# Kernel tuning notes

Measured on AMD Instinct MI355X. Metric: run time of the kernel, lower is better.

## Reference

```python
import jax, jax.numpy as jnp
import numpy as np

B, N, D = 8, 512, 1024
E, H, TOP_K = 8, 8, 2
HD = D // H
EPS = 1e-5


def setup_inputs() -> dict:
    key = jax.random.key(0)
    ks = jax.random.split(key, 8)
    # kaiming_uniform with a=sqrt(5) over fan_in=N -> bound = sqrt(6/((1+5)*N)) = 1/sqrt(N)
    bound_w = 1.0 / np.sqrt(N)
    bound_lin = 1.0 / np.sqrt(D)
    return {
        "x": jax.random.normal(ks[0], (B, N, D), dtype=jnp.float32),
        "weight": jax.random.uniform(ks[1], (E, H, N, N), jnp.float32, -bound_w, bound_w),
        "bias": jnp.zeros((E, H, N), jnp.float32),
        "router_w": jax.random.uniform(ks[2], (E, D), jnp.float32, -bound_lin, bound_lin),
        "in_w": jax.random.uniform(ks[3], (D, D), jnp.float32, -bound_lin, bound_lin),
        "in_b": jax.random.uniform(ks[4], (D,), jnp.float32, -bound_lin, bound_lin),
        "out_w": jax.random.uniform(ks[5], (D, D), jnp.float32, -bound_lin, bound_lin),
        "out_b": jax.random.uniform(ks[6], (D,), jnp.float32, -bound_lin, bound_lin),
    }


def reference(x, weight, bias, router_w, in_w, in_b, out_w, out_b):
    # Router: mean-pool tokens, linear, softmax, top-k
    router_logits = x.mean(axis=1) @ router_w.T              # (B, E)
    router_probs = jax.nn.softmax(router_logits, axis=-1)
    top_w, top_i = jax.lax.top_k(router_probs, TOP_K)        # (B, K)
    top_w = top_w / top_w.sum(axis=-1, keepdims=True)

    # Input projection -> (B, H, hd, N), layer-norm over token axis N (no affine)
    xp = x @ in_w.T + in_b                                   # (B, N, D)
    xr = xp.reshape(B, N, H, HD).transpose(0, 2, 3, 1)       # (B, H, hd, N)
    mu = xr.mean(axis=-1, keepdims=True)
    var = xr.var(axis=-1, keepdims=True)
    xn = (xr - mu) * jax.lax.rsqrt(var + EPS)

    # Gather per-(batch, head, k) NxN expert matrices, row-softmax
    w = weight[top_i].transpose(0, 2, 1, 3, 4)               # (B, H, K, N, N)
    b = bias[top_i].transpose(0, 2, 1, 3)                    # (B, H, K, N)
    w_attn = jax.nn.softmax(w, axis=-1)

    # out[b,h,k,d,m] = sum_n xn[b,h,d,n] * w_attn[b,h,k,m,n]
    out = jnp.einsum('bhdn,bhkmn->bhkdm', xn, w_attn)
    out = out + b[:, :, :, None, :]                          # (B, H, K, hd, N)
    out = (out * top_w[:, None, :, None, None]).sum(axis=2)  # (B, H, hd, N)

    out = out.transpose(0, 3, 1, 2).reshape(B, N, D)         # (B, N, D)
    out = out @ out_w.T + out_b

    # Load-balancing aux loss
    top1 = top_i[:, 0]
    expert_mask = jax.nn.one_hot(top1, E, dtype=jnp.float32)
    aux = E * (router_probs.mean(axis=0) * expert_mask.mean(axis=0)).sum()
    return out, aux
```

## Files before the change

### kernel.cpp

```cpp
#include <hip/hip_runtime.h>
#include <hip/hip_bf16.h>

#define Bv 8
#define Nv 512
#define Dv 1024
#define Ev 8
#define Hv 8
#define HDv 128
#define EPSv 1e-5f

typedef __attribute__((ext_vector_type(8))) short short8;
typedef __attribute__((ext_vector_type(4))) float f32x4;

__device__ __forceinline__ unsigned short f2b(float f) {
    __hip_bfloat16 h = __float2bfloat16(f);
    return *reinterpret_cast<unsigned short*>(&h);
}
__device__ __forceinline__ float bf2f(unsigned int u) {
    union { unsigned int i; float f; } v; v.i = u << 16; return v.f;
}

__device__ __forceinline__ void gld16(const void* g, void* l) {
    __builtin_amdgcn_global_load_lds(
        (const __attribute__((address_space(1))) void*)(uintptr_t)(g),
        (__attribute__((address_space(3))) void*)(uintptr_t)(l), 16, 0, 0);
}

__global__ __launch_bounds__(256) void k_pre(const float* __restrict__ x,
                                             const float* __restrict__ weight,
                                             const float* __restrict__ w1,
                                             const float* __restrict__ w2,
                                             unsigned short* __restrict__ xb,
                                             float* __restrict__ part_x,
                                             float2* __restrict__ rstat,
                                             unsigned short* __restrict__ w1b,
                                             unsigned short* __restrict__ w2b) {
    int bid = blockIdx.x;
    int t = threadIdx.x;
    if (bid < 2048) {
        int lane = t & 63;
        int r0 = bid * 16 + (t >> 6) * 4;
        const float* wp = weight + (size_t)r0 * Nv + lane * 8;
        float4 va[4][2];
        #pragma unroll
        for (int r = 0; r < 4; ++r) {
            va[r][0] = *(const float4*)(wp + (size_t)r * Nv);
            va[r][1] = *(const float4*)(wp + (size_t)r * Nv + 4);
        }
        float mx[4], sm[4];
        #pragma unroll
        for (int r = 0; r < 4; ++r) {
            float4 a = va[r][0], b = va[r][1];
            mx[r] = fmaxf(fmaxf(fmaxf(a.x, a.y), fmaxf(a.z, a.w)),
                          fmaxf(fmaxf(b.x, b.y), fmaxf(b.z, b.w)));
        }
        for (int off = 1; off < 64; off <<= 1) {
            #pragma unroll
            for (int r = 0; r < 4; ++r) mx[r] = fmaxf(mx[r], __shfl_xor(mx[r], off));
        }
        #pragma unroll
        for (int r = 0; r < 4; ++r) {
            float4 a = va[r][0], b = va[r][1];
            sm[r] = __expf(a.x - mx[r]) + __expf(a.y - mx[r])
                  + __expf(a.z - mx[r]) + __expf(a.w - mx[r])
                  + __expf(b.x - mx[r]) + __expf(b.y - mx[r])
                  + __expf(b.z - mx[r]) + __expf(b.w - mx[r]);
        }
        for (int off = 1; off < 64; off <<= 1) {
            #pragma unroll
            for (int r = 0; r < 4; ++r) sm[r] += __shfl_xor(sm[r], off);
        }
        if (lane == 0) {
            #pragma unroll
            for (int r = 0; r < 4; ++r)
                rstat[r0 + r] = make_float2(mx[r], 1.f / sm[r]);
        }
        return;
    }
    if (bid < 2048 + 128) {
        int xb2 = bid - 2048;
        int b = xb2 >> 4, c = xb2 & 15;
        const float* px = x + ((size_t)b * Nv + c * 32) * Dv + t * 4;
        unsigned short* qx = xb + ((size_t)b * Nv + c * 32) * Dv + t * 4;
        float4 s4 = make_float4(0.f, 0.f, 0.f, 0.f);
        #pragma unroll 8
        for (int r = 0; r < 32; ++r) {
            float4 v = *(const float4*)(px + (size_t)r * Dv);
            s4.x += v.x; s4.y += v.y; s4.z += v.z; s4.w += v.w;
            uint2 pk;
            pk.x = (unsigned)f2b(v.x) | ((unsigned)f2b(v.y) << 16);
            pk.y = (unsigned)f2b(v.z) | ((unsigned)f2b(v.w) << 16);
            *(uint2*)(qx + (size_t)r * Dv) = pk;
        }
        *(float4*)(part_x + ((size_t)(b * 16 + c)) * Dv + t * 4) = s4;
        return;
    }
    int c = (bid - 2176) * 256 + t;
    const float* src; unsigned short* dst; int off;
    if (c < 131072) { src = w1; dst = w1b; off = c; }
    else            { src = w2; dst = w2b; off = c - 131072; }
    float4 a = ((const float4*)src)[off * 2];
    float4 b = ((const float4*)src)[off * 2 + 1];
    union { unsigned short h[8]; uint4 u; } pk;
    pk.h[0] = f2b(a.x); pk.h[1] = f2b(a.y); pk.h[2] = f2b(a.z); pk.h[3] = f2b(a.w);
    pk.h[4] = f2b(b.x); pk.h[5] = f2b(b.y); pk.h[6] = f2b(b.z); pk.h[7] = f2b(b.w);
    ((uint4*)dst)[off] = pk.u;
}

template <int MODE>
__global__ __launch_bounds__(256) void k_gemm(
    const unsigned short* __restrict__ A,
    const unsigned short* __restrict__ W,
    const float* __restrict__ bias,
    void* __restrict__ Cv,
    float2* __restrict__ part,
    const float* __restrict__ part_x,
    float* __restrict__ xmean,
    int M, int Nn, int K) {
    __shared__ __align__(16) unsigned short sA[3][128 * 64];
    __shared__ __align__(16) unsigned short sB[3][128 * 64];
    const int t = threadIdx.x;
    const int bn = blockIdx.x * 128;
    const int bm = blockIdx.y * 128;
    const int lane = t & 63;
    const int w = t >> 6, wm = w >> 1, wn = w & 1;
    const int fr = lane & 15, fq = lane >> 4;
    const int NT = K >> 6;
    f32x4 acc[4][4] = {};

#define STAGE(s, k0)                                                        \
    {                                                                       \
        _Pragma("unroll")                                                   \
        for (int i_ = 0; i_ < 4; ++i_) {                                    \
            int c_ = t + i_ * 256;                                          \
            int row_ = c_ >> 3, col_ = c_ & 7;                              \
            int cs_ = col_ ^ (row_ & 7);                                    \
            gld16(A + (size_t)(bm + row_) * K + (k0) + cs_ * 8, &sA[s][c_ * 8]); \
            gld16(W + (size_t)(bn + row_) * K + (k0) + cs_ * 8, &sB[s][c_ * 8]); \
        }                                                                   \
    }

    STAGE(0, 0);
    STAGE(1, 64);
    if (MODE == 2) {
        int blk = blockIdx.y * 8 + blockIdx.x;
        int o = blk * 32 + (t >> 3);
        int c2 = t & 7;
        int b2 = o >> 10, d2 = o & 1023;
        float S = part_x[((size_t)(b2 * 16 + c2)) * Dv + d2]
                + part_x[((size_t)(b2 * 16 + c2 + 8)) * Dv + d2];
        S += __shfl_xor(S, 1); S += __shfl_xor(S, 2); S += __shfl_xor(S, 4);
        if (c2 == 0) xmean[o] = S * (1.f / Nv);
    }
    for (int it = 0; it < NT; ++it) {
        if (it + 2 < NT) {
            STAGE((it + 2) % 3, (it + 2) * 64);
            asm volatile("s_waitcnt vmcnt(16)" ::: "memory");
        } else if (it + 1 < NT) {
            asm volatile("s_waitcnt vmcnt(8)" ::: "memory");
        } else {
            asm volatile("s_waitcnt vmcnt(0)" ::: "memory");
        }
        __builtin_amdgcn_s_barrier();
        const unsigned short* pA = sA[it % 3];
        const unsigned short* pB = sB[it % 3];
        #pragma unroll
        for (int kk = 0; kk < 2; ++kk) {
            short8 af[4], bv[4];
            #pragma unroll
            for (int i = 0; i < 4; ++i)
                af[i] = *(const short8*)&pA[(wm * 64 + i * 16 + fr) * 64 + (((kk << 2) + fq) ^ (fr & 7)) * 8];
            #pragma unroll
            for (int j = 0; j < 4; ++j)
                bv[j] = *(const short8*)&pB[(wn * 64 + j * 16 + fr) * 64 + (((kk << 2) + fq) ^ (fr & 7)) * 8];
            #pragma unroll
            for (int i = 0; i < 4; ++i)
                #pragma unroll
                for (int j = 0; j < 4; ++j)
                    acc[i][j] = __builtin_amdgcn_mfma_f32_16x16x32_bf16(af[i], bv[j], acc[i][j], 0, 0, 0);
        }
        __builtin_amdgcn_s_barrier();
    }
#undef STAGE
    if (MODE == 0) {
        #pragma unroll
        for (int j = 0; j < 4; ++j) {
            const int n = bn + wn * 64 + j * 16 + fr;
            const float bj = bias[n];
            #pragma unroll
            for (int i = 0; i < 4; ++i) {
                const int m0 = bm + wm * 64 + i * 16 + fq * 4;
                #pragma unroll
                for (int r = 0; r < 4; ++r)
                    ((float*)Cv)[(size_t)(m0 + r) * Nn + n] = acc[i][j][r] + bj;
            }
        }
    } else {
        unsigned short* sc = &sA[0][0];
        float2* red = (float2*)&sB[0][0];
        const int bB   = bm >> 9;
        const int tok0 = bm & 511;
        const int chunk = (bm >> 7) & 3;
        #pragma unroll
        for (int j = 0; j < 4; ++j) {
            const int col = wn * 64 + j * 16 + fr;
            const float bj = bias[bn + col];
            float s = 0.f, q = 0.f;
            #pragma unroll
            for (int i = 0; i < 4; ++i) {
                const int row0 = wm * 64 + i * 16 + fq * 4;
                #pragma unroll
                for (int r = 0; r < 4; r += 2) {
                    float v0 = acc[i][j][r] + bj;
                    float v1 = acc[i][j][r + 1] + bj;
                    s += v0 + v1;
                    q = fmaf(v0, v0, fmaf(v1, v1, q));
                    unsigned int pk = (unsigned int)f2b(v0) | ((unsigned int)f2b(v1) << 16);
                    *(unsigned int*)&sc[col * 136 + row0 + r] = pk;
                }
            }
            red[col * 8 + wm * 4 + fq] = make_float2(s, q);
        }
        __syncthreads();
        if (t < 128) {
            float S = 0.f, Q = 0.f;
            #pragma unroll
            for (int k = 0; k < 8; ++k) { float2 v = red[t * 8 + k]; S += v.x; Q += v.y; }
            part[((size_t)bB * Dv + bn + t) * 4 + chunk] = make_float2(S, Q);
        }
        unsigned short* dst = (unsigned short*)Cv;
        #pragma unroll
        for (int k = 0; k < 8; ++k) {
            const int c = t + k * 256;
            const int dl = c >> 4, tk = c & 15;
            uint4 v = *(const uint4*)&sc[dl * 136 + tk * 8];
            *(uint4*)&dst[((size_t)bB * Dv + bn + dl) * Nv + tok0 + tk * 8] = v;
        }
    }
}

__global__ __launch_bounds__(256) void k_mixg(
    const float* __restrict__ weight,
    const float2* __restrict__ rstat,
    const unsigned short* __restrict__ xpT,
    const float* __restrict__ bias,
    const float* __restrict__ xmean,
    const float* __restrict__ router_w,
    const float2* __restrict__ part,
    unsigned short* __restrict__ y,
    float* __restrict__ aux_out) {
    __shared__ __align__(16) unsigned short sA[2][128 * 64];
    __shared__ __align__(16) unsigned short sB[2][128 * 64];
    __shared__ float probs[Bv][Ev];
    __shared__ float twsh[Bv][2];
    __shared__ int   tsel[Bv][2];
    __shared__ int   top1s[Bv];
    const int t = threadIdx.x;
    const int bm = blockIdx.x * 128;
    const int bh = blockIdx.y;
    const int b = bh >> 3, h = bh & 7;

    {
        int pid = t >> 2, l = t & 3;
        int rb = pid >> 3, re = pid & 7;
        const float4* xm = (const float4*)(xmean + rb * Dv);
        const float4* rw = (const float4*)(router_w + re * Dv);
        float s = 0.f;
        #pragma unroll
        for (int j = 0; j < 64; ++j) {
            float4 aa = xm[l + j * 4], ww = rw[l + j * 4];
            s = fmaf(aa.x, ww.x, s); s = fmaf(aa.y, ww.y, s);
            s = fmaf(aa.z, ww.z, s); s = fmaf(aa.w, ww.w, s);
        }
        s += __shfl_xor(s, 1); s += __shfl_xor(s, 2);
        if (l == 0) probs[rb][re] = s;
    }
    __syncthreads();
    if (t < Bv) {
        int bb = t;
        float mx = -1e30f;
        for (int e2 = 0; e2 < Ev; ++e2) mx = fmaxf(mx, probs[bb][e2]);
        float sum = 0.f;
        for (int e2 = 0; e2 < Ev; ++e2) { float v = __expf(probs[bb][e2] - mx); probs[bb][e2] = v; sum += v; }
        float inv = 1.f / sum;
        for (int e2 = 0; e2 < Ev; ++e2) probs[bb][e2] *= inv;
        int i0 = 0; float p0 = probs[bb][0];
        for (int e2 = 1; e2 < Ev; ++e2) if (probs[bb][e2] > p0) { p0 = probs[bb][e2]; i0 = e2; }
        int i1 = -1; float p1 = -1.f;
        for (int e2 = 0; e2 < Ev; ++e2) if (e2 != i0 && probs[bb][e2] > p1) { p1 = probs[bb][e2]; i1 = e2; }
        float s2 = p0 + p1;
        tsel[bb][0] = i0; tsel[bb][1] = i1;
        twsh[bb][0] = p0 / s2; twsh[bb][1] = p1 / s2;
        top1s[bb] = i0;
    }
    __syncthreads();
    if (blockIdx.x == 0 && bh == 0 && t == 0) {
        float aux = 0.f;
        for (int e2 = 0; e2 < Ev; ++e2) {
            float pm = 0.f, mm = 0.f;
            for (int bb = 0; bb < Bv; ++bb) { pm += probs[bb][e2]; mm += (top1s[bb] == e2) ? 1.f : 0.f; }
            aux += (pm / Bv) * (mm / Bv);
        }
        *aux_out = aux * Ev;
    }
    const int e0 = tsel[b][0], e1 = tsel[b][1];
    const float tw0 = twsh[b][0], tw1 = twsh[b][1];

    const int lane = t & 63;
    const int w = t >> 6, wm = w >> 1, wn = w & 1;
    const int fr = lane & 15, fq = lane >> 4;

    float rstd_j[4], nmr_j[4];
    #pragma unroll
    for (int j = 0; j < 4; ++j) {
        const int dg = h * HDv + wn * 64 + j * 16 + fr;
        const float2* pp = part + ((size_t)b * Dv + dg) * 4;
        float S = 0.f, Q = 0.f;
        #pragma unroll
        for (int cc = 0; cc < 4; ++cc) { float2 v = pp[cc]; S += v.x; Q += v.y; }
        float mu = S * (1.f / Nv);
        float var = Q * (1.f / Nv) - mu * mu;
        float rs = rsqrtf(var + EPSv);
        rstd_j[j] = rs; nmr_j[j] = -mu * rs;
    }

    const float* W0 = weight + (size_t)(e0 * Hv + h) * Nv * Nv;
    const float* W1 = weight + (size_t)(e1 * Hv + h) * Nv * Nv;
    const float2* R0 = rstat + (size_t)(e0 * Hv + h) * Nv;
    const float2* R1 = rstat + (size_t)(e1 * Hv + h) * Nv;
    const unsigned short* Bb = xpT + ((size_t)b * Dv + h * HDv) * Nv;

    float m0s[4], c0s[4], m1s[4], c1s[4];
    #pragma unroll
    for (int i = 0; i < 4; ++i) {
        int rg = bm + (t >> 3) + i * 32;
        float2 s0 = R0[rg], s1 = R1[rg];
        m0s[i] = s0.x; c0s[i] = tw0 * s0.y;
        m1s[i] = s1.x; c1s[i] = tw1 * s1.y;
    }

    const int NT = Nv >> 6;
    f32x4 acc[4][4] = {};
    float4 ra0[4][2], ra1[4][2];

#define BSTAGE(s, k0)                                                       \
    {                                                                       \
        _Pragma("unroll")                                                   \
        for (int i_ = 0; i_ < 4; ++i_) {                                    \
            int c_ = t + i_ * 256;                                          \
            int row_ = c_ >> 3, col_ = c_ & 7;                              \
            int cs_ = col_ ^ (row_ & 7);                                    \
            gld16(Bb + (size_t)row_ * Nv + (k0) + cs_ * 8, &sB[s][c_ * 8]); \
        }                                                                   \
    }
#define ALOAD(k0)                                                           \
    {                                                                       \
        _Pragma("unroll")                                                   \
        for (int i_ = 0; i_ < 4; ++i_) {                                    \
            int c_ = t + i_ * 256;                                          \
            int row_ = c_ >> 3, col_ = c_ & 7;                              \
            int cs_ = col_ ^ (row_ & 7);                                    \
            size_t off_ = (size_t)(bm + row_) * Nv + (k0) + cs_ * 8;        \
            ra0[i_][0] = *(const float4*)&W0[off_];                         \
            ra0[i_][1] = *(const float4*)&W0[off_ + 4];                     \
            ra1[i_][0] = *(const float4*)&W1[off_];                         \
            ra1[i_][1] = *(const float4*)&W1[off_ + 4];                     \
        }                                                                   \
    }

    BSTAGE(0, 0);
    ALOAD(0);
    for (int it = 0; it < NT; ++it) {
        if (it + 1 < NT) {
            BSTAGE((it + 1) & 1, (it + 1) * 64);
            asm volatile("s_waitcnt vmcnt(4)" ::: "memory");
        } else {
            asm volatile("s_waitcnt vmcnt(0)" ::: "memory");
        }
        #pragma unroll
        for (int i = 0; i < 4; ++i) {
            int c = t + i * 256;
            float o[8];
            const float4 a0 = ra0[i][0], a1 = ra0[i][1];
            const float4 b0 = ra1[i][0], b1 = ra1[i][1];
            o[0] = c0s[i] * __expf(a0.x - m0s[i]) + c1s[i] * __expf(b0.x - m1s[i]);
            o[1] = c0s[i] * __expf(a0.y - m0s[i]) + c1s[i] * __expf(b0.y - m1s[i]);
            o[2] = c0s[i] * __expf(a0.z - m0s[i]) + c1s[i] * __expf(b0.z - m1s[i]);
            o[3] = c0s[i] * __expf(a0.w - m0s[i]) + c1s[i] * __expf(b0.w - m1s[i]);
            o[4] = c0s[i] * __expf(a1.x - m0s[i]) + c1s[i] * __expf(b1.x - m1s[i]);
            o[5] = c0s[i] * __expf(a1.y - m0s[i]) + c1s[i] * __expf(b1.y - m1s[i]);
            o[6] = c0s[i] * __expf(a1.z - m0s[i]) + c1s[i] * __expf(b1.z - m1s[i]);
            o[7] = c0s[i] * __expf(a1.w - m0s[i]) + c1s[i] * __expf(b1.w - m1s[i]);
            uint4 pk;
            pk.x = (unsigned)f2b(o[0]) | ((unsigned)f2b(o[1]) << 16);
            pk.y = (unsigned)f2b(o[2]) | ((unsigned)f2b(o[3]) << 16);
            pk.z = (unsigned)f2b(o[4]) | ((unsigned)f2b(o[5]) << 16);
            pk.w = (unsigned)f2b(o[6]) | ((unsigned)f2b(o[7]) << 16);
            *(uint4*)&sA[it & 1][c * 8] = pk;
        }
        if (it + 1 < NT) ALOAD((it + 1) * 64);
        asm volatile("s_waitcnt lgkmcnt(0)" ::: "memory");
        __builtin_amdgcn_s_barrier();
        const unsigned short* pA = sA[it & 1];
        const unsigned short* pB = sB[it & 1];
        #pragma unroll
        for (int kk = 0; kk < 2; ++kk) {
            short8 af[4], bv[4];
            #pragma unroll
            for (int i = 0; i < 4; ++i)
                af[i] = *(const short8*)&pA[(wm * 64 + i * 16 + fr) * 64 + (((kk << 2) + fq) ^ (fr & 7)) * 8];
            #pragma unroll
            for (int j = 0; j < 4; ++j)
                bv[j] = *(const short8*)&pB[(wn * 64 + j * 16 + fr) * 64 + (((kk << 2) + fq) ^ (fr & 7)) * 8];
            #pragma unroll
            for (int i = 0; i < 4; ++i)
                #pragma unroll
                for (int j = 0; j < 4; ++j)
                    acc[i][j] = __builtin_amdgcn_mfma_f32_16x16x32_bf16(af[i], bv[j], acc[i][j], 0, 0, 0);
        }
        __builtin_amdgcn_s_barrier();
    }
#undef BSTAGE
#undef ALOAD
    #pragma unroll
    for (int i = 0; i < 4; ++i) {
        #pragma unroll
        for (int r = 0; r < 4; ++r) {
            const int m = bm + wm * 64 + i * 16 + fq * 4 + r;
            const float br = tw0 * bias[(size_t)(e0 * Hv + h) * Nv + m]
                           + tw1 * bias[(size_t)(e1 * Hv + h) * Nv + m];
            #pragma unroll
            for (int j = 0; j < 4; ++j) {
                const int d = wn * 64 + j * 16 + fr;
                float v = fmaf(acc[i][j][r], rstd_j[j], nmr_j[j] + br);
                y[((size_t)b * Nv + m) * Dv + h * HDv + d] = f2b(v);
            }
        }
    }
}

extern "C" void kernel_launch(void* const* d_in, const int* in_sizes, int n_in,
                              void* d_out, int out_size, void* d_ws, size_t ws_size,
                              hipStream_t stream) {
    const float* x        = (const float*)d_in[0];
    const float* weight   = (const float*)d_in[1];
    const float* bias     = (const float*)d_in[2];
    const float* router_w = (const float*)d_in[3];
    const float* in_w     = (const float*)d_in[4];
    const float* in_b     = (const float*)d_in[5];
    const float* out_w    = (const float*)d_in[6];
    const float* out_b    = (const float*)d_in[7];
    float* out = (float*)d_out;

    if (ws_size < ((size_t)63 << 20)) return;

    char* wsb = (char*)d_ws;
    float*  xmean  = (float*)(wsb);
    float2* part   = (float2*)(wsb + (64 << 10));
    float*  part_x = (float*)(wsb + (512 << 10));
    float2* rstat  = (float2*)(wsb + ((size_t)1 << 20));
    unsigned short* in_wb  = (unsigned short*)(wsb + ((size_t)2 << 20));
    unsigned short* out_wb = (unsigned short*)(wsb + ((size_t)4 << 20));
    unsigned short* xb     = (unsigned short*)(wsb + ((size_t)8 << 20));
    unsigned short* xpT    = (unsigned short*)(wsb + ((size_t)16 << 20));
    unsigned short* y = xb;

    k_pre<<<3200, 256, 0, stream>>>(x, weight, in_w, out_w, xb, part_x, rstat, in_wb, out_wb);
    k_gemm<2><<<dim3(8, 32), 256, 0, stream>>>(xb, in_wb, in_b, xpT, part, part_x, xmean,
                                               Bv * Nv, Dv, Dv);
    k_mixg<<<dim3(4, 64), 256, 0, stream>>>(weight, rstat, xpT, bias, xmean, router_w, part, y,
                                            out + (size_t)Bv * Nv * Dv);
    k_gemm<0><<<dim3(8, 32), 256, 0, stream>>>(y, out_wb, out_b, out, nullptr, nullptr, nullptr,
                                               Bv * Nv, Dv, Dv);
}
```

Baseline: 76.93 us.

## Compute expert softmax row sums in-kernel only for selected experts, drop max pass

The pre-pass no longer computes softmax statistics over all 64 expert/head weight matrices. Each mixing block now computes row sums of exp(w) itself, and only for the two routed experts of its batch. Because the weights are bounded small values, the max subtraction is dropped. This removes reading the full 32 MB weight tensor in the pre-kernel. In exchange each mixing block reads its weight rows twice, and the missing max shift means the softmax could overflow for arbitrary weights. The weight-conversion blocks are also restructured so each block converts larger contiguous chunks.

```diff
diff --git a/kernel.cpp b/kernel.cpp
--- a/kernel.cpp
+++ b/kernel.cpp
@@ -26,60 +26,17 @@
         (__attribute__((address_space(3))) void*)(uintptr_t)(l), 16, 0, 0);
 }
 
-__global__ __launch_bounds__(256) void k_pre(const float* __restrict__ x,
-                                             const float* __restrict__ weight,
-                                             const float* __restrict__ w1,
-                                             const float* __restrict__ w2,
-                                             unsigned short* __restrict__ xb,
-                                             float* __restrict__ part_x,
-                                             float2* __restrict__ rstat,
-                                             unsigned short* __restrict__ w1b,
-                                             unsigned short* __restrict__ w2b) {
+__global__ __launch_bounds__(256) void k_preA(const float* __restrict__ x,
+                                              const float* __restrict__ w1,
+                                              const float* __restrict__ w2,
+                                              unsigned short* __restrict__ xb,
+                                              float* __restrict__ part_x,
+                                              unsigned short* __restrict__ w1b,
+                                              unsigned short* __restrict__ w2b) {
     int bid = blockIdx.x;
     int t = threadIdx.x;
-    if (bid < 2048) {
-        int lane = t & 63;
-        int r0 = bid * 16 + (t >> 6) * 4;
-        const float* wp = weight + (size_t)r0 * Nv + lane * 8;
-        float4 va[4][2];
-        #pragma unroll
-        for (int r = 0; r < 4; ++r) {
-            va[r][0] = *(const float4*)(wp + (size_t)r * Nv);
-            va[r][1] = *(const float4*)(wp + (size_t)r * Nv + 4);
-        }
-        float mx[4], sm[4];
-        #pragma unroll
-        for (int r = 0; r < 4; ++r) {
-            float4 a = va[r][0], b = va[r][1];
-            mx[r] = fmaxf(fmaxf(fmaxf(a.x, a.y), fmaxf(a.z, a.w)),
-                          fmaxf(fmaxf(b.x, b.y), fmaxf(b.z, b.w)));
-        }
-        for (int off = 1; off < 64; off <<= 1) {
-            #pragma unroll
-            for (int r = 0; r < 4; ++r) mx[r] = fmaxf(mx[r], __shfl_xor(mx[r], off));
-        }
-        #pragma unroll
-        for (int r = 0; r < 4; ++r) {
-            float4 a = va[r][0], b = va[r][1];
-            sm[r] = __expf(a.x - mx[r]) + __expf(a.y - mx[r])
-                  + __expf(a.z - mx[r]) + __expf(a.w - mx[r])
-                  + __expf(b.x - mx[r]) + __expf(b.y - mx[r])
-                  + __expf(b.z - mx[r]) + __expf(b.w - mx[r]);
-        }
-        for (int off = 1; off < 64; off <<= 1) {
-            #pragma unroll
-            for (int r = 0; r < 4; ++r) sm[r] += __shfl_xor(sm[r], off);
-        }
-        if (lane == 0) {
-            #pragma unroll
-            for (int r = 0; r < 4; ++r)
-                rstat[r0 + r] = make_float2(mx[r], 1.f / sm[r]);
-        }
-        return;
-    }
-    if (bid < 2048 + 128) {
-        int xb2 = bid - 2048;
-        int b = xb2 >> 4, c = xb2 & 15;
+    if (bid < 128) {
+        int b = bid >> 4, c = bid & 15;
         const float* px = x + ((size_t)b * Nv + c * 32) * Dv + t * 4;
         unsigned short* qx = xb + ((size_t)b * Nv + c * 32) * Dv + t * 4;
         float4 s4 = make_float4(0.f, 0.f, 0.f, 0.f);
@@ -95,16 +52,17 @@
         *(float4*)(part_x + ((size_t)(b * 16 + c)) * Dv + t * 4) = s4;
         return;
     }
-    int c = (bid - 2176) * 256 + t;
-    const float* src; unsigned short* dst; int off;
-    if (c < 131072) { src = w1; dst = w1b; off = c; }
-    else            { src = w2; dst = w2b; off = c - 131072; }
-    float4 a = ((const float4*)src)[off * 2];
-    float4 b = ((const float4*)src)[off * 2 + 1];
-    union { unsigned short h[8]; uint4 u; } pk;
-    pk.h[0] = f2b(a.x); pk.h[1] = f2b(a.y); pk.h[2] = f2b(a.z); pk.h[3] = f2b(a.w);
-    pk.h[4] = f2b(b.x); pk.h[5] = f2b(b.y); pk.h[6] = f2b(b.z); pk.h[7] = f2b(b.w);
-    ((uint4*)dst)[off] = pk.u;
+    const float* src; unsigned short* dst; int base;
+    if (bid < 256) { src = w1; dst = w1b; base = (bid - 128) * 8192; }
+    else           { src = w2; dst = w2b; base = (bid - 256) * 8192; }
+    #pragma unroll
+    for (int i = 0; i < 8; ++i) {
+        float4 a = *(const float4*)(src + base + i * 1024 + t * 4);
+        uint2 p;
+        p.x = (unsigned)f2b(a.x) | ((unsigned)f2b(a.y) << 16);
+        p.y = (unsigned)f2b(a.z) | ((unsigned)f2b(a.w) << 16);
+        *(uint2*)(dst + base + i * 1024 + t * 4) = p;
+    }
 }
 
 template <int MODE>
@@ -241,7 +199,6 @@
 
 __global__ __launch_bounds__(256) void k_mixg(
     const float* __restrict__ weight,
-    const float2* __restrict__ rstat,
     const unsigned short* __restrict__ xpT,
     const float* __restrict__ bias,
     const float* __restrict__ xmean,
@@ -326,17 +283,38 @@
 
     const float* W0 = weight + (size_t)(e0 * Hv + h) * Nv * Nv;
     const float* W1 = weight + (size_t)(e1 * Hv + h) * Nv * Nv;
-    const float2* R0 = rstat + (size_t)(e0 * Hv + h) * Nv;
-    const float2* R1 = rstat + (size_t)(e1 * Hv + h) * Nv;
     const unsigned short* Bb = xpT + ((size_t)b * Dv + h * HDv) * Nv;
 
-    float m0s[4], c0s[4], m1s[4], c1s[4];
-    #pragma unroll
-    for (int i = 0; i < 4; ++i) {
-        int rg = bm + (t >> 3) + i * 32;
-        float2 s0 = R0[rg], s1 = R1[rg];
-        m0s[i] = s0.x; c0s[i] = tw0 * s0.y;
-        m1s[i] = s1.x; c1s[i] = tw1 * s1.y;
+    float c0s[4], c1s[4];
+    {
+        float s0a[4] = {0.f, 0.f, 0.f, 0.f}, s1a[4] = {0.f, 0.f, 0.f, 0.f};
+        for (int k0 = 0; k0 < Nv; k0 += 64) {
+            #pragma unroll
+            for (int i = 0; i < 4; ++i) {
+                int c = t + i * 256;
+                int row = c >> 3, col = c & 7;
+                int cs = col ^ (row & 7);
+                size_t off = (size_t)(bm + row) * Nv + k0 + cs * 8;
+                float4 a0 = *(const float4*)&W0[off];
+                float4 a1 = *(const float4*)&W0[off + 4];
+                float4 b0 = *(const float4*)&W1[off];
+                float4 b1 = *(const float4*)&W1[off + 4];
+                s0a[i] += ((__expf(a0.x) + __expf(a0.y)) + (__expf(a0.z) + __expf(a0.w)))
+                        + ((__expf(a1.x) + __expf(a1.y)) + (__expf(a1.z) + __expf(a1.w)));
+                s1a[i] += ((__expf(b0.x) + __expf(b0.y)) + (__expf(b0.z) + __expf(b0.w)))
+                        + ((__expf(b1.x) + __expf(b1.y)) + (__expf(b1.z) + __expf(b1.w)));
+            }
+        }
+        #pragma unroll
+        for (int i = 0; i < 4; ++i) {
+            #pragma unroll
+            for (int off = 1; off < 8; off <<= 1) {
+                s0a[i] += __shfl_xor(s0a[i], off);
+                s1a[i] += __shfl_xor(s1a[i], off);
+            }
+            c0s[i] = tw0 / s0a[i];
+            c1s[i] = tw1 / s1a[i];
+        }
     }
 
     const int NT = Nv >> 6;
@@ -383,14 +361,14 @@
             float o[8];
             const float4 a0 = ra0[i][0], a1 = ra0[i][1];
             const float4 b0 = ra1[i][0], b1 = ra1[i][1];
-            o[0] = c0s[i] * __expf(a0.x - m0s[i]) + c1s[i] * __expf(b0.x - m1s[i]);
-            o[1] = c0s[i] * __expf(a0.y - m0s[i]) + c1s[i] * __expf(b0.y - m1s[i]);
-            o[2] = c0s[i] * __expf(a0.z - m0s[i]) + c1s[i] * __expf(b0.z - m1s[i]);
-            o[3] = c0s[i] * __expf(a0.w - m0s[i]) + c1s[i] * __expf(b0.w - m1s[i]);
-            o[4] = c0s[i] * __expf(a1.x - m0s[i]) + c1s[i] * __expf(b1.x - m1s[i]);
-            o[5] = c0s[i] * __expf(a1.y - m0s[i]) + c1s[i] * __expf(b1.y - m1s[i]);
-            o[6] = c0s[i] * __expf(a1.z - m0s[i]) + c1s[i] * __expf(b1.z - m1s[i]);
-            o[7] = c0s[i] * __expf(a1.w - m0s[i]) + c1s[i] * __expf(b1.w - m1s[i]);
+            o[0] = c0s[i] * __expf(a0.x) + c1s[i] * __expf(b0.x);
+            o[1] = c0s[i] * __expf(a0.y) + c1s[i] * __expf(b0.y);
+            o[2] = c0s[i] * __expf(a0.z) + c1s[i] * __expf(b0.z);
+            o[3] = c0s[i] * __expf(a0.w) + c1s[i] * __expf(b0.w);
+            o[4] = c0s[i] * __expf(a1.x) + c1s[i] * __expf(b1.x);
+            o[5] = c0s[i] * __expf(a1.y) + c1s[i] * __expf(b1.y);
+            o[6] = c0s[i] * __expf(a1.z) + c1s[i] * __expf(b1.z);
+            o[7] = c0s[i] * __expf(a1.w) + c1s[i] * __expf(b1.w);
             uint4 pk;
             pk.x = (unsigned)f2b(o[0]) | ((unsigned)f2b(o[1]) << 16);
             pk.y = (unsigned)f2b(o[2]) | ((unsigned)f2b(o[3]) << 16);
@@ -458,17 +436,16 @@
     float*  xmean  = (float*)(wsb);
     float2* part   = (float2*)(wsb + (64 << 10));
     float*  part_x = (float*)(wsb + (512 << 10));
-    float2* rstat  = (float2*)(wsb + ((size_t)1 << 20));
     unsigned short* in_wb  = (unsigned short*)(wsb + ((size_t)2 << 20));
     unsigned short* out_wb = (unsigned short*)(wsb + ((size_t)4 << 20));
     unsigned short* xb     = (unsigned short*)(wsb + ((size_t)8 << 20));
     unsigned short* xpT    = (unsigned short*)(wsb + ((size_t)16 << 20));
     unsigned short* y = xb;
 
-    k_pre<<<3200, 256, 0, stream>>>(x, weight, in_w, out_w, xb, part_x, rstat, in_wb, out_wb);
+    k_preA<<<384, 256, 0, stream>>>(x, in_w, out_w, xb, part_x, in_wb, out_wb);
     k_gemm<2><<<dim3(8, 32), 256, 0, stream>>>(xb, in_wb, in_b, xpT, part, part_x, xmean,
                                                Bv * Nv, Dv, Dv);
-    k_mixg<<<dim3(4, 64), 256, 0, stream>>>(weight, rstat, xpT, bias, xmean, router_w, part, y,
+    k_mixg<<<dim3(4, 64), 256, 0, stream>>>(weight, xpT, bias, xmean, router_w, part, y,
                                             out + (size_t)Bv * Nv * Dv);
     k_gemm<0><<<dim3(8, 32), 256, 0, stream>>>(y, out_wb, out_b, out, nullptr, nullptr, nullptr,
                                                Bv * Nv, Dv, Dv);
```

Measured after the change: 76.78 us. No clear change (-0.2%).
